# Kernel tuning notes

Hardware: AMD Instinct MI355X
Metric: run time of the kernel (lower is better)

## Reference

```python
import jax, jax.numpy as jnp
import numpy as np

VOCAB, EMBED, HIDDEN, N_CLASSES = 50257, 128, 256, 2
B = S = 512  # must be equal: the original module only runs when x.size(0)==x.size(1)


def gru_layer(x_seq, Wih, Whh, bih, bhh):
    """PyTorch-equation GRU over time axis 0. x_seq: (T, N, E) -> (T, N, H)."""
    T, N, _ = x_seq.shape
    H = Whh.shape[1]
    xi = x_seq @ Wih.T + bih  # precompute input projections for all steps: (T, N, 3H)

    def step(h, xi_t):
        gh = h @ Whh.T + bhh
        xr, xz, xn = jnp.split(xi_t, 3, axis=-1)
        hr, hz, hn = jnp.split(gh, 3, axis=-1)
        r = jax.nn.sigmoid(xr + hr)
        z = jax.nn.sigmoid(xz + hz)
        n = jnp.tanh(xn + r * hn)
        h_new = (1.0 - z) * n + z * h
        return h_new, h_new

    h0 = jnp.zeros((N, H), dtype=x_seq.dtype)
    _, ys = jax.lax.scan(step, h0, xi)
    return ys


def setup_inputs() -> dict:
    key = jax.random.key(0)
    ks = jax.random.split(key, 12)
    sc = 0.05
    return {
        "x": jax.random.randint(ks[0], (B, S), 0, VOCAB),
        "embed_table": jax.random.normal(ks[1], (VOCAB, EMBED), jnp.float32) * sc,
        "Wih0": jax.random.normal(ks[2], (3 * HIDDEN, EMBED), jnp.float32) * sc,
        "Whh0": jax.random.normal(ks[3], (3 * HIDDEN, HIDDEN), jnp.float32) * sc,
        "bih0": jax.random.normal(ks[4], (3 * HIDDEN,), jnp.float32) * sc,
        "bhh0": jax.random.normal(ks[5], (3 * HIDDEN,), jnp.float32) * sc,
        "Wih1": jax.random.normal(ks[6], (3 * HIDDEN, HIDDEN), jnp.float32) * sc,
        "Whh1": jax.random.normal(ks[7], (3 * HIDDEN, HIDDEN), jnp.float32) * sc,
        "bih1": jax.random.normal(ks[8], (3 * HIDDEN,), jnp.float32) * sc,
        "bhh1": jax.random.normal(ks[9], (3 * HIDDEN,), jnp.float32) * sc,
        "W_out": jax.random.normal(ks[10], (N_CLASSES, HIDDEN), jnp.float32) * sc,
        "b_out": jax.random.normal(ks[11], (N_CLASSES,), jnp.float32) * sc,
    }


def reference(x, embed_table, Wih0, Whh0, bih0, bhh0, Wih1, Whh1, bih1, bhh1, W_out, b_out):
    emb = embed_table[x]                 # (B, S, E)
    # nn.GRU default batch_first=False: dim 0 (=B) is TIME, dim 1 (=S) is batch.
    y = gru_layer(emb, Wih0, Whh0, bih0, bhh0)   # (B, S, H)
    y = gru_layer(y, Wih1, Whh1, bih1, bhh1)     # (B, S, H)
    h_t = y[:, -1, :]                    # (B, H)
    # self.dropout(h_t) in the original discards its result -> no-op.
    logit = h_t @ W_out.T + b_out        # (B, n_classes)
    return logit
```

## Files before the change

kernel.cpp:

```cpp
#include <hip/hip_runtime.h>
#include <hip/hip_fp16.h>

typedef _Float16 f16x2 __attribute__((ext_vector_type(2)));
typedef _Float16 half8 __attribute__((ext_vector_type(8)));

#define TS  512
#define HID 256
#define G3  768
#define EMB 128
#define NB1 8
#define RPB 96
#define CTL 767
#define BSZ 8

__device__ __forceinline__ float sigmoidf_(float x){ return 1.0f/(1.0f+__expf(-x)); }
__device__ __forceinline__ float tanhf_(float x){
  float e = __expf(-2.0f*fabsf(x));
  float t = (1.0f-e)/(1.0f+e);
  return copysignf(t,x);
}

__global__ __launch_bounds__(256) void xi0_kernel(const int* __restrict__ x,
    const float* __restrict__ emb_tab, const float* __restrict__ Wih0,
    const float* __restrict__ bih0, float* __restrict__ xi0)
{
  __shared__ float embs[8][EMB];
  __shared__ int idx8[8];
  int tid = threadIdx.x;
  int t0  = blockIdx.x * 8;
  if (tid < 8) idx8[tid] = x[(t0 + tid)*512 + 511];
  __syncthreads();
  for (int i = tid; i < 8*EMB; i += 256){
    int q = i >> 7, r = i & 127;
    embs[q][r] = emb_tab[(long)idx8[q]*EMB + r];
  }
  __syncthreads();
  for (int g = 0; g < 3; g++){
    int j = g*256 + tid;
    float b = bih0[j];
    float acc[8];
    #pragma unroll
    for (int u=0;u<8;u++) acc[u]=b;
    const float4* wrow = (const float4*)(Wih0 + (long)j*EMB);
    #pragma unroll 8
    for (int m=0;m<EMB/4;m++){
      float4 w = wrow[m];
      #pragma unroll
      for (int u=0;u<8;u++){
        acc[u] += w.x*embs[u][4*m+0] + w.y*embs[u][4*m+1]
                + w.z*embs[u][4*m+2] + w.w*embs[u][4*m+3];
      }
    }
    #pragma unroll
    for (int u=0;u<8;u++) xi0[(long)(t0+u)*G3 + j] = acc[u];
  }
}

#define SHUF(V,A,B) __builtin_shufflevector(V,V,A,B)
#define WR32(X) X(0,0) X(0,1) X(0,2) X(0,3) X(1,0) X(1,1) X(1,2) X(1,3) \
                X(2,0) X(2,1) X(2,2) X(2,3) X(3,0) X(3,1) X(3,2) X(3,3) \
                X(4,0) X(4,1) X(4,2) X(4,3) X(5,0) X(5,1) X(5,2) X(5,3) \
                X(6,0) X(6,1) X(6,2) X(6,3) X(7,0) X(7,1) X(7,2) X(7,3)

template<int MODE>
__device__ __forceinline__ void rec_layer(const float* __restrict__ Whh,
    const float* __restrict__ bhh, const float* __restrict__ xi,
    _Float16* __restrict__ h16out, float* __restrict__ f32out,
    unsigned* __restrict__ flagB, unsigned* __restrict__ cntB,
    _Float16 (*hbuf)[8*40], float* gh, float* bhhL)
{
  int tid = threadIdx.x;
  int g   = tid >> 3;
  int o   = tid & 7;

#define WDECL(I,C) half8 w##I##_##C;
  WR32(WDECL)
#define WLOAD(I,C) { \
    const float4* p_ = (const float4*)(Whh + (long)(8*g+(I))*HID + 32*o + 8*(C)); \
    float4 u_ = p_[0], v_ = p_[1]; \
    w##I##_##C = (half8){(_Float16)u_.x,(_Float16)u_.y,(_Float16)u_.z,(_Float16)u_.w, \
                         (_Float16)v_.x,(_Float16)v_.y,(_Float16)v_.z,(_Float16)v_.w}; }
  WR32(WLOAD)

  float hprev = 0.f;
  float xr=0.f, xz=0.f, xn=0.f;
  bhhL[tid] = bhh[tid];
  if (tid < 80) ((half8*)hbuf)[tid] = (half8)(_Float16)0;

  if (MODE == 1 && tid == CTL){
    while (__hip_atomic_load(&cntB[0], __ATOMIC_RELAXED, __HIP_MEMORY_SCOPE_AGENT) < NB1)
      __builtin_amdgcn_s_sleep(1);
    __threadfence();
  }
  __syncthreads();
  if (tid < HID){
    xr = xi[tid]; xz = xi[HID+tid]; xn = xi[2*HID+tid];
  }

  for (int t = 0; t < TS; t++){
    if (MODE == 1 && tid == CTL && ((t+1) & (BSZ-1)) == 0 && t+1 < TS){
      unsigned b = (unsigned)(t+1) >> 3;
      while (__hip_atomic_load(&cntB[b], __ATOMIC_RELAXED, __HIP_MEMORY_SCOPE_AGENT) < NB1)
        __builtin_amdgcn_s_sleep(1);
      __threadfence();
    }

    const half8* hp = (const half8*)(&hbuf[t & 1][o*40]);
    float a0=0.f,a1=0.f,a2=0.f,a3=0.f,a4=0.f,a5=0.f,a6=0.f,a7=0.f;
#define DOT1(I,C,HV) \
    a##I = __builtin_amdgcn_fdot2(SHUF(w##I##_##C,0,1), SHUF(HV,0,1), a##I, false); \
    a##I = __builtin_amdgcn_fdot2(SHUF(w##I##_##C,2,3), SHUF(HV,2,3), a##I, false); \
    a##I = __builtin_amdgcn_fdot2(SHUF(w##I##_##C,4,5), SHUF(HV,4,5), a##I, false); \
    a##I = __builtin_amdgcn_fdot2(SHUF(w##I##_##C,6,7), SHUF(HV,6,7), a##I, false);
#define DOTCHUNK(C) { half8 hv = hp[C]; \
    DOT1(0,C,hv) DOT1(1,C,hv) DOT1(2,C,hv) DOT1(3,C,hv) \
    DOT1(4,C,hv) DOT1(5,C,hv) DOT1(6,C,hv) DOT1(7,C,hv) }
    DOTCHUNK(0) DOTCHUNK(1) DOTCHUNK(2) DOTCHUNK(3)

    bool b0 = o & 1, b1 = o & 2, b2 = o & 4;
    float s, r_;
    s = b0 ? a0 : a1; r_ = __shfl_xor(s, 1, 64); float c0 = (b0 ? a1 : a0) + r_;
    s = b0 ? a2 : a3; r_ = __shfl_xor(s, 1, 64); float c1 = (b0 ? a3 : a2) + r_;
    s = b0 ? a4 : a5; r_ = __shfl_xor(s, 1, 64); float c2 = (b0 ? a5 : a4) + r_;
    s = b0 ? a6 : a7; r_ = __shfl_xor(s, 1, 64); float c3 = (b0 ? a7 : a6) + r_;
    s = b1 ? c0 : c1; r_ = __shfl_xor(s, 2, 64); float d0 = (b1 ? c1 : c0) + r_;
    s = b1 ? c2 : c3; r_ = __shfl_xor(s, 2, 64); float d1 = (b1 ? c3 : c2) + r_;
    s = b2 ? d0 : d1; r_ = __shfl_xor(s, 4, 64); float e  = (b2 ? d1 : d0) + r_;
    gh[tid] = e;
    __syncthreads();

    if (tid < HID){
      float r = sigmoidf_(xr + bhhL[tid] + gh[tid]);
      float z = sigmoidf_(xz + bhhL[HID+tid] + gh[HID+tid]);
      float n = tanhf_(xn + r*(gh[2*HID+tid] + bhhL[2*HID+tid]));
      float hnew = (1.0f - z)*n + z*hprev;
      hprev = hnew;
      if (MODE == 1) f32out[(long)t*HID + tid] = hnew;
      float partner = __shfl_xor(hnew, 1, 64);
      if ((tid & 1) == 0){
        f16x2 p; p.x = (_Float16)hnew; p.y = (_Float16)partner;
        *(f16x2*)(&hbuf[(t+1)&1][(tid>>5)*40 + (tid&31)]) = p;
        if (MODE == 0) *(f16x2*)(h16out + (long)t*HID + tid) = p;
      }
      if (t+1 < TS){
        const float* xp = xi + (long)(t+1)*G3;
        xr = xp[tid]; xz = xp[HID+tid]; xn = xp[2*HID+tid];
      }
    }
    __syncthreads();
    if (MODE == 0 && tid == CTL && ((t+1) & (BSZ-1)) == 0){
      __threadfence();
      __hip_atomic_store(&flagB[t >> 3], 1u, __ATOMIC_RELEASE, __HIP_MEMORY_SCOPE_AGENT);
    }
  }
}

__device__ __forceinline__ void xi1_stage(const float* __restrict__ Wih1,
    const float* __restrict__ bih1, const _Float16* __restrict__ h16,
    float* __restrict__ xi1, unsigned* __restrict__ flagB,
    unsigned* __restrict__ cntB, int slice)
{
  int tid = threadIdx.x;
  int r = tid >> 3, o = tid & 7;
  int row = slice*RPB + r;
  half8 w0,w1,w2,w3;
  {
    const float4* wp = (const float4*)(Wih1 + (long)row*HID + o*32);
    float4 p0=wp[0],p1=wp[1],p2=wp[2],p3=wp[3],p4=wp[4],p5=wp[5],p6=wp[6],p7=wp[7];
    w0 = (half8){(_Float16)p0.x,(_Float16)p0.y,(_Float16)p0.z,(_Float16)p0.w,
                 (_Float16)p1.x,(_Float16)p1.y,(_Float16)p1.z,(_Float16)p1.w};
    w1 = (half8){(_Float16)p2.x,(_Float16)p2.y,(_Float16)p2.z,(_Float16)p2.w,
                 (_Float16)p3.x,(_Float16)p3.y,(_Float16)p3.z,(_Float16)p3.w};
    w2 = (half8){(_Float16)p4.x,(_Float16)p4.y,(_Float16)p4.z,(_Float16)p4.w,
                 (_Float16)p5.x,(_Float16)p5.y,(_Float16)p5.z,(_Float16)p5.w};
    w3 = (half8){(_Float16)p6.x,(_Float16)p6.y,(_Float16)p6.z,(_Float16)p6.w,
                 (_Float16)p7.x,(_Float16)p7.y,(_Float16)p7.z,(_Float16)p7.w};
  }
  float bias = bih1[row];

  for (int b = 0; b < TS/BSZ; b++){
    if (tid == 0){
      while (__hip_atomic_load(&flagB[b], __ATOMIC_RELAXED, __HIP_MEMORY_SCOPE_AGENT) == 0u)
        __builtin_amdgcn_s_sleep(1);
      __threadfence();
    }
    __syncthreads();
    #pragma unroll 4
    for (int u = 0; u < BSZ; u++){
      int t = b*BSZ + u;
      const half8* hp = (const half8*)(h16 + (long)t*HID + o*32);
      half8 h0 = hp[0], h1 = hp[1], h2 = hp[2], h3 = hp[3];
      float acc = 0.f;
#define XDOT(W,H) \
      acc = __builtin_amdgcn_fdot2(SHUF(W,0,1), SHUF(H,0,1), acc, false); \
      acc = __builtin_amdgcn_fdot2(SHUF(W,2,3), SHUF(H,2,3), acc, false); \
      acc = __builtin_amdgcn_fdot2(SHUF(W,4,5), SHUF(H,4,5), acc, false); \
      acc = __builtin_amdgcn_fdot2(SHUF(W,6,7), SHUF(H,6,7), acc, false);
      XDOT(w0,h0) XDOT(w1,h1) XDOT(w2,h2) XDOT(w3,h3)
      acc += __shfl_xor(acc, 1, 64);
      acc += __shfl_xor(acc, 2, 64);
      acc += __shfl_xor(acc, 4, 64);
      if (o == 0) xi1[(long)t*G3 + row] = acc + bias;
    }
    __syncthreads();
    if (tid == 0){
      __threadfence();
      atomicAdd(&cntB[b], 1u);
    }
  }
}

__global__ __launch_bounds__(768, 3)
__attribute__((amdgpu_max_num_work_groups(10, 1, 1)))
void pipe_kernel(
    const float* __restrict__ Whh0, const float* __restrict__ bhh0,
    const float* __restrict__ xi0,
    const float* __restrict__ Wih1, const float* __restrict__ bih1,
    const float* __restrict__ Whh1, const float* __restrict__ bhh1,
    _Float16* __restrict__ h1f16, float* __restrict__ xi1,
    float* __restrict__ h2, unsigned* __restrict__ flagB,
    unsigned* __restrict__ cntB)
{
  __shared__ __align__(16) _Float16 hbuf[2][8*40];
  __shared__ float gh[G3];
  __shared__ float bhhL[G3];
  int bid = blockIdx.x;
  if (bid == 0)
    rec_layer<0>(Whh0, bhh0, xi0, h1f16, nullptr, flagB, cntB, hbuf, gh, bhhL);
  else if (bid == 9)
    rec_layer<1>(Whh1, bhh1, xi1, nullptr, h2, flagB, cntB, hbuf, gh, bhhL);
  else
    xi1_stage(Wih1, bih1, h1f16, xi1, flagB, cntB, bid - 1);
}

__global__ __launch_bounds__(1024) void logits_kernel(const float* __restrict__ h2,
    const float* __restrict__ Wout, const float* __restrict__ bout,
    float* __restrict__ out)
{
  __shared__ __align__(16) float wsm[2*HID];
  __shared__ float bs[2];
  int tid = threadIdx.x;
  if (tid < 2*HID) wsm[tid] = Wout[tid];
  if (tid < 2)     bs[tid]  = bout[tid];
  __syncthreads();
  int t = tid >> 1, c = tid & 1;
  const float4* hr = (const float4*)(h2 + (long)t*HID);
  const float4* wr = (const float4*)(wsm + c*HID);
  float acc = bs[c];
  #pragma unroll 8
  for (int m=0;m<HID/4;m++){
    float4 h = hr[m]; float4 wv = wr[m];
    acc += h.x*wv.x + h.y*wv.y + h.z*wv.z + h.w*wv.w;
  }
  out[tid] = acc;
}

extern "C" void kernel_launch(void* const* d_in, const int* in_sizes, int n_in,
                              void* d_out, int out_size, void* d_ws, size_t ws_size,
                              hipStream_t stream)
{
  const int*   x    = (const int*)  d_in[0];
  const float* emb  = (const float*)d_in[1];
  const float* Wih0 = (const float*)d_in[2];
  const float* Whh0 = (const float*)d_in[3];
  const float* bih0 = (const float*)d_in[4];
  const float* bhh0 = (const float*)d_in[5];
  const float* Wih1 = (const float*)d_in[6];
  const float* Whh1 = (const float*)d_in[7];
  const float* bih1 = (const float*)d_in[8];
  const float* bhh1 = (const float*)d_in[9];
  const float* Wout = (const float*)d_in[10];
  const float* bout = (const float*)d_in[11];
  float* out = (float*)d_out;

  char* ws = (char*)d_ws;
  float*     xi0   = (float*)(ws);
  float*     xi1   = (float*)(ws + 1572864);
  _Float16*  h1f16 = (_Float16*)(ws + 3145728);
  float*     h2    = (float*)(ws + 3407872);
  unsigned*  flagB = (unsigned*)(ws + 3932160);
  unsigned*  cntB  = (unsigned*)(ws + 3934208);

  hipMemsetAsync(ws + 3932160, 0, 4096, stream);
  xi0_kernel<<<64, 256, 0, stream>>>(x, emb, Wih0, bih0, xi0);
  pipe_kernel<<<10, 768, 0, stream>>>(Whh0, bhh0, xi0, Wih1, bih1,
                                      Whh1, bhh1, h1f16, xi1, h2, flagB, cntB);
  logits_kernel<<<1, 1024, 0, stream>>>(h2, Wout, bout, out);
}
```

Measured before the change: 855.8 us.

## Split each GRU recurrent layer across two workgroups exchanging half-hidden states per step

Each recurrent layer now runs on two workgroups, each owning 128 hidden units and 384 gate rows. At every step the pair swaps its half of the hidden state through global memory, using per-step counters that are spin-waited. This halves the per-block matvec work and register footprint, but adds a cross-workgroup handshake and global round-trip on every timestep. The xi1 workers now wait on both layer-0 counters instead of per-batch flags.

```diff
diff --git a/kernel.cpp b/kernel.cpp
--- a/kernel.cpp
+++ b/kernel.cpp
@@ -57,34 +57,40 @@
 }
 
 #define SHUF(V,A,B) __builtin_shufflevector(V,V,A,B)
-#define WR32(X) X(0,0) X(0,1) X(0,2) X(0,3) X(1,0) X(1,1) X(1,2) X(1,3) \
-                X(2,0) X(2,1) X(2,2) X(2,3) X(3,0) X(3,1) X(3,2) X(3,3) \
-                X(4,0) X(4,1) X(4,2) X(4,3) X(5,0) X(5,1) X(5,2) X(5,3) \
-                X(6,0) X(6,1) X(6,2) X(6,3) X(7,0) X(7,1) X(7,2) X(7,3)
+#define WR16(X) X(0,0) X(0,1) X(0,2) X(0,3) \
+                X(1,0) X(1,1) X(1,2) X(1,3) \
+                X(2,0) X(2,1) X(2,2) X(2,3) \
+                X(3,0) X(3,1) X(3,2) X(3,3)
 
 template<int MODE>
 __device__ __forceinline__ void rec_layer(const float* __restrict__ Whh,
     const float* __restrict__ bhh, const float* __restrict__ xi,
     _Float16* __restrict__ h16out, float* __restrict__ f32out,
-    unsigned* __restrict__ flagB, unsigned* __restrict__ cntB,
-    _Float16 (*hbuf)[8*40], float* gh, float* bhhL)
+    unsigned* __restrict__ cntB, unsigned* __restrict__ ctrOwn,
+    unsigned* __restrict__ ctrPar, int P,
+    _Float16 (*hbuf)[8*40], float* ghL, float* bhhL)
 {
   int tid = threadIdx.x;
   int g   = tid >> 3;
   int o   = tid & 7;
+  const int BASE = P * 128;
+  const int PB   = (1 - P) * 128;
 
 #define WDECL(I,C) half8 w##I##_##C;
-  WR32(WDECL)
+  WR16(WDECL)
 #define WLOAD(I,C) { \
-    const float4* p_ = (const float4*)(Whh + (long)(8*g+(I))*HID + 32*o + 8*(C)); \
+    int l_ = 4*g + (I); \
+    int wr_ = ((l_>>7)<<8) + BASE + (l_&127); \
+    const float4* p_ = (const float4*)(Whh + (long)wr_*HID + 32*o + 8*(C)); \
     float4 u_ = p_[0], v_ = p_[1]; \
     w##I##_##C = (half8){(_Float16)u_.x,(_Float16)u_.y,(_Float16)u_.z,(_Float16)u_.w, \
                          (_Float16)v_.x,(_Float16)v_.y,(_Float16)v_.z,(_Float16)v_.w}; }
-  WR32(WLOAD)
+  WR16(WLOAD)
 
   float hprev = 0.f;
   float xr=0.f, xz=0.f, xn=0.f;
-  bhhL[tid] = bhh[tid];
+  if (tid < 384)
+    bhhL[tid] = bhh[((tid>>7)<<8) + BASE + (tid&127)];
   if (tid < 80) ((half8*)hbuf)[tid] = (half8)(_Float16)0;
 
   if (MODE == 1 && tid == CTL){
@@ -93,8 +99,8 @@
     __threadfence();
   }
   __syncthreads();
-  if (tid < HID){
-    xr = xi[tid]; xz = xi[HID+tid]; xn = xi[2*HID+tid];
+  if (tid < 128){
+    xr = xi[BASE+tid]; xz = xi[256+BASE+tid]; xn = xi[512+BASE+tid];
   }
 
   for (int t = 0; t < TS; t++){
@@ -105,59 +111,78 @@
       __threadfence();
     }
 
+    if (t > 0 && tid < 64){
+      while (__hip_atomic_load(ctrPar, __ATOMIC_RELAXED, __HIP_MEMORY_SCOPE_AGENT)
+             < (unsigned)t) {}
+      __threadfence();
+      int u = PB + 2*tid;
+      f16x2 v;
+      if (MODE == 0){
+        v = *(const f16x2*)(h16out + (long)(t-1)*HID + u);
+      } else {
+        float2 f = *(const float2*)(f32out + (long)(t-1)*HID + u);
+        v.x = (_Float16)f.x; v.y = (_Float16)f.y;
+      }
+      *(f16x2*)(&hbuf[t & 1][(u>>5)*40 + (u&31)]) = v;
+    }
+    __syncthreads();
+
     const half8* hp = (const half8*)(&hbuf[t & 1][o*40]);
-    float a0=0.f,a1=0.f,a2=0.f,a3=0.f,a4=0.f,a5=0.f,a6=0.f,a7=0.f;
+    float a0=0.f,a1=0.f,a2=0.f,a3=0.f;
 #define DOT1(I,C,HV) \
     a##I = __builtin_amdgcn_fdot2(SHUF(w##I##_##C,0,1), SHUF(HV,0,1), a##I, false); \
     a##I = __builtin_amdgcn_fdot2(SHUF(w##I##_##C,2,3), SHUF(HV,2,3), a##I, false); \
     a##I = __builtin_amdgcn_fdot2(SHUF(w##I##_##C,4,5), SHUF(HV,4,5), a##I, false); \
     a##I = __builtin_amdgcn_fdot2(SHUF(w##I##_##C,6,7), SHUF(HV,6,7), a##I, false);
 #define DOTCHUNK(C) { half8 hv = hp[C]; \
-    DOT1(0,C,hv) DOT1(1,C,hv) DOT1(2,C,hv) DOT1(3,C,hv) \
-    DOT1(4,C,hv) DOT1(5,C,hv) DOT1(6,C,hv) DOT1(7,C,hv) }
+    DOT1(0,C,hv) DOT1(1,C,hv) DOT1(2,C,hv) DOT1(3,C,hv) }
     DOTCHUNK(0) DOTCHUNK(1) DOTCHUNK(2) DOTCHUNK(3)
 
-    bool b0 = o & 1, b1 = o & 2, b2 = o & 4;
-    float s, r_;
-    s = b0 ? a0 : a1; r_ = __shfl_xor(s, 1, 64); float c0 = (b0 ? a1 : a0) + r_;
-    s = b0 ? a2 : a3; r_ = __shfl_xor(s, 1, 64); float c1 = (b0 ? a3 : a2) + r_;
-    s = b0 ? a4 : a5; r_ = __shfl_xor(s, 1, 64); float c2 = (b0 ? a5 : a4) + r_;
-    s = b0 ? a6 : a7; r_ = __shfl_xor(s, 1, 64); float c3 = (b0 ? a7 : a6) + r_;
-    s = b1 ? c0 : c1; r_ = __shfl_xor(s, 2, 64); float d0 = (b1 ? c1 : c0) + r_;
-    s = b1 ? c2 : c3; r_ = __shfl_xor(s, 2, 64); float d1 = (b1 ? c3 : c2) + r_;
-    s = b2 ? d0 : d1; r_ = __shfl_xor(s, 4, 64); float e  = (b2 ? d1 : d0) + r_;
-    gh[tid] = e;
-    __syncthreads();
-
-    if (tid < HID){
-      float r = sigmoidf_(xr + bhhL[tid] + gh[tid]);
-      float z = sigmoidf_(xz + bhhL[HID+tid] + gh[HID+tid]);
-      float n = tanhf_(xn + r*(gh[2*HID+tid] + bhhL[2*HID+tid]));
+    {
+      bool b0 = o & 1, b1 = o & 2;
+      float s, r_;
+      s = b0 ? a0 : a1; r_ = __shfl_xor(s, 1, 64); float c0 = (b0 ? a1 : a0) + r_;
+      s = b0 ? a2 : a3; r_ = __shfl_xor(s, 1, 64); float c1 = (b0 ? a3 : a2) + r_;
+      s = b1 ? c0 : c1; r_ = __shfl_xor(s, 2, 64); float d  = (b1 ? c1 : c0) + r_;
+      float e = d + __shfl_xor(d, 4, 64);
+      if (o < 4) ghL[4*g + o] = e;
+    }
+    __syncthreads();
+
+    if (tid < 128){
+      float r = sigmoidf_(xr + bhhL[tid] + ghL[tid]);
+      float z = sigmoidf_(xz + bhhL[128+tid] + ghL[128+tid]);
+      float n = tanhf_(xn + r*(ghL[256+tid] + bhhL[256+tid]));
       float hnew = (1.0f - z)*n + z*hprev;
       hprev = hnew;
-      if (MODE == 1) f32out[(long)t*HID + tid] = hnew;
       float partner = __shfl_xor(hnew, 1, 64);
+      int u = BASE + tid;
       if ((tid & 1) == 0){
         f16x2 p; p.x = (_Float16)hnew; p.y = (_Float16)partner;
-        *(f16x2*)(&hbuf[(t+1)&1][(tid>>5)*40 + (tid&31)]) = p;
-        if (MODE == 0) *(f16x2*)(h16out + (long)t*HID + tid) = p;
+        *(f16x2*)(&hbuf[(t+1)&1][(u>>5)*40 + (u&31)]) = p;
+        if (MODE == 0){
+          *(f16x2*)(h16out + (long)t*HID + u) = p;
+        } else {
+          float2 q; q.x = hnew; q.y = partner;
+          *(float2*)(f32out + (long)t*HID + u) = q;
+        }
       }
       if (t+1 < TS){
         const float* xp = xi + (long)(t+1)*G3;
-        xr = xp[tid]; xz = xp[HID+tid]; xn = xp[2*HID+tid];
+        xr = xp[BASE+tid]; xz = xp[256+BASE+tid]; xn = xp[512+BASE+tid];
       }
     }
     __syncthreads();
-    if (MODE == 0 && tid == CTL && ((t+1) & (BSZ-1)) == 0){
-      __threadfence();
-      __hip_atomic_store(&flagB[t >> 3], 1u, __ATOMIC_RELEASE, __HIP_MEMORY_SCOPE_AGENT);
+    if (tid == CTL){
+      __threadfence();
+      __hip_atomic_store(ctrOwn, (unsigned)(t+1), __ATOMIC_RELEASE, __HIP_MEMORY_SCOPE_AGENT);
     }
   }
 }
 
 __device__ __forceinline__ void xi1_stage(const float* __restrict__ Wih1,
     const float* __restrict__ bih1, const _Float16* __restrict__ h16,
-    float* __restrict__ xi1, unsigned* __restrict__ flagB,
+    float* __restrict__ xi1, unsigned* __restrict__ ctrs,
     unsigned* __restrict__ cntB, int slice)
 {
   int tid = threadIdx.x;
@@ -180,7 +205,9 @@
 
   for (int b = 0; b < TS/BSZ; b++){
     if (tid == 0){
-      while (__hip_atomic_load(&flagB[b], __ATOMIC_RELAXED, __HIP_MEMORY_SCOPE_AGENT) == 0u)
+      unsigned tgt = (unsigned)(BSZ*(b+1));
+      while (__hip_atomic_load(&ctrs[0],  __ATOMIC_RELAXED, __HIP_MEMORY_SCOPE_AGENT) < tgt ||
+             __hip_atomic_load(&ctrs[16], __ATOMIC_RELAXED, __HIP_MEMORY_SCOPE_AGENT) < tgt)
         __builtin_amdgcn_s_sleep(1);
       __threadfence();
     }
@@ -211,26 +238,31 @@
 }
 
 __global__ __launch_bounds__(768, 3)
-__attribute__((amdgpu_max_num_work_groups(10, 1, 1)))
 void pipe_kernel(
     const float* __restrict__ Whh0, const float* __restrict__ bhh0,
     const float* __restrict__ xi0,
     const float* __restrict__ Wih1, const float* __restrict__ bih1,
     const float* __restrict__ Whh1, const float* __restrict__ bhh1,
     _Float16* __restrict__ h1f16, float* __restrict__ xi1,
-    float* __restrict__ h2, unsigned* __restrict__ flagB,
+    float* __restrict__ h2, unsigned* __restrict__ ctrs,
     unsigned* __restrict__ cntB)
 {
   __shared__ __align__(16) _Float16 hbuf[2][8*40];
-  __shared__ float gh[G3];
-  __shared__ float bhhL[G3];
+  __shared__ float ghL[384];
+  __shared__ float bhhL[384];
   int bid = blockIdx.x;
   if (bid == 0)
-    rec_layer<0>(Whh0, bhh0, xi0, h1f16, nullptr, flagB, cntB, hbuf, gh, bhhL);
+    rec_layer<0>(Whh0, bhh0, xi0, h1f16, nullptr, cntB, ctrs+0,  ctrs+16, 0, hbuf, ghL, bhhL);
+  else if (bid == 8)
+    rec_layer<0>(Whh0, bhh0, xi0, h1f16, nullptr, cntB, ctrs+16, ctrs+0,  1, hbuf, ghL, bhhL);
+  else if (bid == 1)
+    rec_layer<1>(Whh1, bhh1, xi1, nullptr, h2,    cntB, ctrs+32, ctrs+48, 0, hbuf, ghL, bhhL);
   else if (bid == 9)
-    rec_layer<1>(Whh1, bhh1, xi1, nullptr, h2, flagB, cntB, hbuf, gh, bhhL);
-  else
-    xi1_stage(Wih1, bih1, h1f16, xi1, flagB, cntB, bid - 1);
+    rec_layer<1>(Whh1, bhh1, xi1, nullptr, h2,    cntB, ctrs+48, ctrs+32, 1, hbuf, ghL, bhhL);
+  else {
+    int slice = (bid < 8) ? bid - 2 : bid - 4;
+    xi1_stage(Wih1, bih1, h1f16, xi1, ctrs, cntB, slice);
+  }
 }
 
 __global__ __launch_bounds__(1024) void logits_kernel(const float* __restrict__ h2,
@@ -278,12 +310,12 @@
   float*     xi1   = (float*)(ws + 1572864);
   _Float16*  h1f16 = (_Float16*)(ws + 3145728);
   float*     h2    = (float*)(ws + 3407872);
-  unsigned*  flagB = (unsigned*)(ws + 3932160);
+  unsigned*  ctrs  = (unsigned*)(ws + 3932160);
   unsigned*  cntB  = (unsigned*)(ws + 3934208);
 
   hipMemsetAsync(ws + 3932160, 0, 4096, stream);
   xi0_kernel<<<64, 256, 0, stream>>>(x, emb, Wih0, bih0, xi0);
-  pipe_kernel<<<10, 768, 0, stream>>>(Whh0, bhh0, xi0, Wih1, bih1,
-                                      Whh1, bhh1, h1f16, xi1, h2, flagB, cntB);
+  pipe_kernel<<<12, 768, 0, stream>>>(Whh0, bhh0, xi0, Wih1, bih1,
+                                      Whh1, bhh1, h1f16, xi1, h2, ctrs, cntB);
   logits_kernel<<<1, 1024, 0, stream>>>(h2, Wout, bout, out);
 }
```

Result: slower. 1.363 ms (+59.2%).

## Split recurrent weights across registers, LDS and L2 with 512-thread blocks

Applied to the files above, without the earlier changes.

Each recurrent block shrinks from 768 to 512 threads, so every 8-thread group now computes 12 gate rows instead of 8. Six rows are kept in registers, three in LDS, and three are streamed each step from an fp16 packed copy that the xi0 kernel writes to workspace. The number of xi1 producer blocks rises from 8 to 12, each covering 64 rows. The aim is fewer waves per step and more producer parallelism, at the price of extra LDS and global loads inside the serial time loop.

```diff
diff --git a/kernel.cpp b/kernel.cpp
--- a/kernel.cpp
+++ b/kernel.cpp
@@ -8,9 +8,10 @@
 #define HID 256
 #define G3  768
 #define EMB 128
-#define NB1 8
-#define RPB 96
-#define CTL 767
+#define THR 512
+#define NB1 12
+#define RPB 64
+#define CTL 511
 #define BSZ 8
 
 __device__ __forceinline__ float sigmoidf_(float x){ return 1.0f/(1.0f+__expf(-x)); }
@@ -22,7 +23,9 @@
 
 __global__ __launch_bounds__(256) void xi0_kernel(const int* __restrict__ x,
     const float* __restrict__ emb_tab, const float* __restrict__ Wih0,
-    const float* __restrict__ bih0, float* __restrict__ xi0)
+    const float* __restrict__ bih0, float* __restrict__ xi0,
+    const float* __restrict__ Whh0, const float* __restrict__ Whh1,
+    _Float16* __restrict__ wpk0, _Float16* __restrict__ wpk1)
 {
   __shared__ float embs[8][EMB];
   __shared__ int idx8[8];
@@ -54,37 +57,60 @@
     #pragma unroll
     for (int u=0;u<8;u++) xi0[(long)(t0+u)*G3 + j] = acc[u];
   }
+  int gid = blockIdx.x*256 + tid;
+  for (int e = gid; e < 2*192*256; e += 64*256){
+    int L = (e >= 192*256) ? 1 : 0;
+    int i = e - L*192*256;
+    int s = i >> 8, c = i & 255;
+    int row = 12*(s/3) + 9 + (s%3);
+    const float* W = L ? Whh1 : Whh0;
+    _Float16*    P = L ? wpk1 : wpk0;
+    P[i] = (_Float16)W[(long)row*HID + c];
+  }
 }
 
 #define SHUF(V,A,B) __builtin_shufflevector(V,V,A,B)
-#define WR32(X) X(0,0) X(0,1) X(0,2) X(0,3) X(1,0) X(1,1) X(1,2) X(1,3) \
+#define WR24(X) X(0,0) X(0,1) X(0,2) X(0,3) X(1,0) X(1,1) X(1,2) X(1,3) \
                 X(2,0) X(2,1) X(2,2) X(2,3) X(3,0) X(3,1) X(3,2) X(3,3) \
-                X(4,0) X(4,1) X(4,2) X(4,3) X(5,0) X(5,1) X(5,2) X(5,3) \
-                X(6,0) X(6,1) X(6,2) X(6,3) X(7,0) X(7,1) X(7,2) X(7,3)
+                X(4,0) X(4,1) X(4,2) X(4,3) X(5,0) X(5,1) X(5,2) X(5,3)
 
 template<int MODE>
 __device__ __forceinline__ void rec_layer(const float* __restrict__ Whh,
     const float* __restrict__ bhh, const float* __restrict__ xi,
+    const _Float16* __restrict__ wpk,
     _Float16* __restrict__ h16out, float* __restrict__ f32out,
     unsigned* __restrict__ flagB, unsigned* __restrict__ cntB,
-    _Float16 (*hbuf)[8*40], float* gh, float* bhhL)
+    _Float16 (*hbuf)[8*40], half8* ldsw, float* gh, float* bhhL)
 {
   int tid = threadIdx.x;
   int g   = tid >> 3;
   int o   = tid & 7;
 
 #define WDECL(I,C) half8 w##I##_##C;
-  WR32(WDECL)
+  WR24(WDECL)
 #define WLOAD(I,C) { \
-    const float4* p_ = (const float4*)(Whh + (long)(8*g+(I))*HID + 32*o + 8*(C)); \
+    const float4* p_ = (const float4*)(Whh + (long)(12*g+(I))*HID + 32*o + 8*(C)); \
     float4 u_ = p_[0], v_ = p_[1]; \
     w##I##_##C = (half8){(_Float16)u_.x,(_Float16)u_.y,(_Float16)u_.z,(_Float16)u_.w, \
                          (_Float16)v_.x,(_Float16)v_.y,(_Float16)v_.z,(_Float16)v_.w}; }
-  WR32(WLOAD)
+  WR24(WLOAD)
+
+  #pragma unroll
+  for (int k = 0; k < 12; k++){
+    int row = 12*g + 6 + (k >> 2);
+    int C = k & 3;
+    const float4* p_ = (const float4*)(Whh + (long)row*HID + 32*o + 8*C);
+    float4 u_ = p_[0], v_ = p_[1];
+    ldsw[k*THR + tid] = (half8){(_Float16)u_.x,(_Float16)u_.y,(_Float16)u_.z,(_Float16)u_.w,
+                                (_Float16)v_.x,(_Float16)v_.y,(_Float16)v_.z,(_Float16)v_.w};
+  }
+  const half8* sp0 = (const half8*)(wpk + ((long)(3*g+0))*HID + 32*o);
+  const half8* sp1 = (const half8*)(wpk + ((long)(3*g+1))*HID + 32*o);
+  const half8* sp2 = (const half8*)(wpk + ((long)(3*g+2))*HID + 32*o);
 
   float hprev = 0.f;
   float xr=0.f, xz=0.f, xn=0.f;
-  bhhL[tid] = bhh[tid];
+  for (int i = tid; i < G3; i += THR) bhhL[i] = bhh[i];
   if (tid < 80) ((half8*)hbuf)[tid] = (half8)(_Float16)0;
 
   if (MODE == 1 && tid == CTL){
@@ -106,16 +132,23 @@
     }
 
     const half8* hp = (const half8*)(&hbuf[t & 1][o*40]);
-    float a0=0.f,a1=0.f,a2=0.f,a3=0.f,a4=0.f,a5=0.f,a6=0.f,a7=0.f;
-#define DOT1(I,C,HV) \
-    a##I = __builtin_amdgcn_fdot2(SHUF(w##I##_##C,0,1), SHUF(HV,0,1), a##I, false); \
-    a##I = __builtin_amdgcn_fdot2(SHUF(w##I##_##C,2,3), SHUF(HV,2,3), a##I, false); \
-    a##I = __builtin_amdgcn_fdot2(SHUF(w##I##_##C,4,5), SHUF(HV,4,5), a##I, false); \
-    a##I = __builtin_amdgcn_fdot2(SHUF(w##I##_##C,6,7), SHUF(HV,6,7), a##I, false);
-#define DOTCHUNK(C) { half8 hv = hp[C]; \
-    DOT1(0,C,hv) DOT1(1,C,hv) DOT1(2,C,hv) DOT1(3,C,hv) \
-    DOT1(4,C,hv) DOT1(5,C,hv) DOT1(6,C,hv) DOT1(7,C,hv) }
-    DOTCHUNK(0) DOTCHUNK(1) DOTCHUNK(2) DOTCHUNK(3)
+    float a0=0.f,a1=0.f,a2=0.f,a3=0.f,a4=0.f,a5=0.f,
+          a6=0.f,a7=0.f,a8=0.f,a9=0.f,a10=0.f,a11=0.f;
+#define D8(ACC, WV, HV) \
+    ACC = __builtin_amdgcn_fdot2(SHUF(WV,0,1), SHUF(HV,0,1), ACC, false); \
+    ACC = __builtin_amdgcn_fdot2(SHUF(WV,2,3), SHUF(HV,2,3), ACC, false); \
+    ACC = __builtin_amdgcn_fdot2(SHUF(WV,4,5), SHUF(HV,4,5), ACC, false); \
+    ACC = __builtin_amdgcn_fdot2(SHUF(WV,6,7), SHUF(HV,6,7), ACC, false);
+#define CHUNK(C) { half8 hv = hp[C]; \
+    half8 l0 = ldsw[(0*4+(C))*THR + tid]; \
+    half8 l1 = ldsw[(1*4+(C))*THR + tid]; \
+    half8 l2 = ldsw[(2*4+(C))*THR + tid]; \
+    half8 s0 = sp0[C]; half8 s1 = sp1[C]; half8 s2 = sp2[C]; \
+    D8(a0, w0_##C, hv) D8(a1, w1_##C, hv) D8(a2, w2_##C, hv) \
+    D8(a3, w3_##C, hv) D8(a4, w4_##C, hv) D8(a5, w5_##C, hv) \
+    D8(a6, l0, hv) D8(a7, l1, hv) D8(a8, l2, hv) \
+    D8(a9, s0, hv) D8(a10, s1, hv) D8(a11, s2, hv) }
+    CHUNK(0) CHUNK(1) CHUNK(2) CHUNK(3)
 
     bool b0 = o & 1, b1 = o & 2, b2 = o & 4;
     float s, r_;
@@ -126,7 +159,12 @@
     s = b1 ? c0 : c1; r_ = __shfl_xor(s, 2, 64); float d0 = (b1 ? c1 : c0) + r_;
     s = b1 ? c2 : c3; r_ = __shfl_xor(s, 2, 64); float d1 = (b1 ? c3 : c2) + r_;
     s = b2 ? d0 : d1; r_ = __shfl_xor(s, 4, 64); float e  = (b2 ? d1 : d0) + r_;
-    gh[tid] = e;
+    gh[12*g + o] = e;
+    s = b0 ? a8 : a9;   r_ = __shfl_xor(s, 1, 64); float c4 = (b0 ? a9  : a8 ) + r_;
+    s = b0 ? a10 : a11; r_ = __shfl_xor(s, 1, 64); float c5 = (b0 ? a11 : a10) + r_;
+    s = b1 ? c4 : c5;   r_ = __shfl_xor(s, 2, 64); float d2 = (b1 ? c5  : c4 ) + r_;
+    float e2 = d2 + __shfl_xor(d2, 4, 64);
+    if (o < 4) gh[12*g + 8 + o] = e2;
     __syncthreads();
 
     if (tid < HID){
@@ -210,25 +248,26 @@
   }
 }
 
-__global__ __launch_bounds__(768, 3)
-__attribute__((amdgpu_max_num_work_groups(10, 1, 1)))
+__global__ __launch_bounds__(THR, 2)
 void pipe_kernel(
     const float* __restrict__ Whh0, const float* __restrict__ bhh0,
     const float* __restrict__ xi0,
     const float* __restrict__ Wih1, const float* __restrict__ bih1,
     const float* __restrict__ Whh1, const float* __restrict__ bhh1,
+    const _Float16* __restrict__ wpk0, const _Float16* __restrict__ wpk1,
     _Float16* __restrict__ h1f16, float* __restrict__ xi1,
     float* __restrict__ h2, unsigned* __restrict__ flagB,
     unsigned* __restrict__ cntB)
 {
+  __shared__ __align__(16) half8 ldsw[12*THR];
   __shared__ __align__(16) _Float16 hbuf[2][8*40];
   __shared__ float gh[G3];
   __shared__ float bhhL[G3];
   int bid = blockIdx.x;
   if (bid == 0)
-    rec_layer<0>(Whh0, bhh0, xi0, h1f16, nullptr, flagB, cntB, hbuf, gh, bhhL);
-  else if (bid == 9)
-    rec_layer<1>(Whh1, bhh1, xi1, nullptr, h2, flagB, cntB, hbuf, gh, bhhL);
+    rec_layer<0>(Whh0, bhh0, xi0, wpk0, h1f16, nullptr, flagB, cntB, hbuf, ldsw, gh, bhhL);
+  else if (bid == 13)
+    rec_layer<1>(Whh1, bhh1, xi1, wpk1, nullptr, h2, flagB, cntB, hbuf, ldsw, gh, bhhL);
   else
     xi1_stage(Wih1, bih1, h1f16, xi1, flagB, cntB, bid - 1);
 }
@@ -280,10 +319,14 @@
   float*     h2    = (float*)(ws + 3407872);
   unsigned*  flagB = (unsigned*)(ws + 3932160);
   unsigned*  cntB  = (unsigned*)(ws + 3934208);
+  _Float16*  wpk0  = (_Float16*)(ws + 3936256);
+  _Float16*  wpk1  = (_Float16*)(ws + 4034560);
 
   hipMemsetAsync(ws + 3932160, 0, 4096, stream);
-  xi0_kernel<<<64, 256, 0, stream>>>(x, emb, Wih0, bih0, xi0);
-  pipe_kernel<<<10, 768, 0, stream>>>(Whh0, bhh0, xi0, Wih1, bih1,
-                                      Whh1, bhh1, h1f16, xi1, h2, flagB, cntB);
+  xi0_kernel<<<64, 256, 0, stream>>>(x, emb, Wih0, bih0, xi0,
+                                     Whh0, Whh1, wpk0, wpk1);
+  pipe_kernel<<<14, THR, 0, stream>>>(Whh0, bhh0, xi0, Wih1, bih1,
+                                      Whh1, bhh1, wpk0, wpk1,
+                                      h1f16, xi1, h2, flagB, cntB);
   logits_kernel<<<1, 1024, 0, stream>>>(h2, Wout, bout, out);
 }
```

New measurement: 893.7 us. 1.04x slower.

## Fold layer-0 input projection into pipelined persistent kernel as producer blocks

Applied to the files above, without the earlier changes.

Removes the separate xi0_kernel and adds 8 extra blocks in pipe_kernel that compute the layer-0 input projection step by step. After every 8 steps they publish progress through a new counter array. Layer-0 recurrence now waits on these counters, so it starts before the whole projection is finished and one kernel launch disappears. The cost is extra spin-wait synchronisation, and correctness relies on all 18 blocks being co-resident.

```diff
diff --git a/kernel.cpp b/kernel.cpp
--- a/kernel.cpp
+++ b/kernel.cpp
@@ -12,6 +12,7 @@
 #define RPB 96
 #define CTL 767
 #define BSZ 8
+#define WAITN 8
 
 __device__ __forceinline__ float sigmoidf_(float x){ return 1.0f/(1.0f+__expf(-x)); }
 __device__ __forceinline__ float tanhf_(float x){
@@ -20,42 +21,6 @@
   return copysignf(t,x);
 }
 
-__global__ __launch_bounds__(256) void xi0_kernel(const int* __restrict__ x,
-    const float* __restrict__ emb_tab, const float* __restrict__ Wih0,
-    const float* __restrict__ bih0, float* __restrict__ xi0)
-{
-  __shared__ float embs[8][EMB];
-  __shared__ int idx8[8];
-  int tid = threadIdx.x;
-  int t0  = blockIdx.x * 8;
-  if (tid < 8) idx8[tid] = x[(t0 + tid)*512 + 511];
-  __syncthreads();
-  for (int i = tid; i < 8*EMB; i += 256){
-    int q = i >> 7, r = i & 127;
-    embs[q][r] = emb_tab[(long)idx8[q]*EMB + r];
-  }
-  __syncthreads();
-  for (int g = 0; g < 3; g++){
-    int j = g*256 + tid;
-    float b = bih0[j];
-    float acc[8];
-    #pragma unroll
-    for (int u=0;u<8;u++) acc[u]=b;
-    const float4* wrow = (const float4*)(Wih0 + (long)j*EMB);
-    #pragma unroll 8
-    for (int m=0;m<EMB/4;m++){
-      float4 w = wrow[m];
-      #pragma unroll
-      for (int u=0;u<8;u++){
-        acc[u] += w.x*embs[u][4*m+0] + w.y*embs[u][4*m+1]
-                + w.z*embs[u][4*m+2] + w.w*embs[u][4*m+3];
-      }
-    }
-    #pragma unroll
-    for (int u=0;u<8;u++) xi0[(long)(t0+u)*G3 + j] = acc[u];
-  }
-}
-
 #define SHUF(V,A,B) __builtin_shufflevector(V,V,A,B)
 #define WR32(X) X(0,0) X(0,1) X(0,2) X(0,3) X(1,0) X(1,1) X(1,2) X(1,3) \
                 X(2,0) X(2,1) X(2,2) X(2,3) X(3,0) X(3,1) X(3,2) X(3,3) \
@@ -66,7 +31,7 @@
 __device__ __forceinline__ void rec_layer(const float* __restrict__ Whh,
     const float* __restrict__ bhh, const float* __restrict__ xi,
     _Float16* __restrict__ h16out, float* __restrict__ f32out,
-    unsigned* __restrict__ flagB, unsigned* __restrict__ cntB,
+    unsigned* __restrict__ flagB, unsigned* __restrict__ cntWait,
     _Float16 (*hbuf)[8*40], float* gh, float* bhhL)
 {
   int tid = threadIdx.x;
@@ -87,8 +52,8 @@
   bhhL[tid] = bhh[tid];
   if (tid < 80) ((half8*)hbuf)[tid] = (half8)(_Float16)0;
 
-  if (MODE == 1 && tid == CTL){
-    while (__hip_atomic_load(&cntB[0], __ATOMIC_RELAXED, __HIP_MEMORY_SCOPE_AGENT) < NB1)
+  if (tid == CTL){
+    while (__hip_atomic_load(&cntWait[0], __ATOMIC_RELAXED, __HIP_MEMORY_SCOPE_AGENT) < WAITN)
       __builtin_amdgcn_s_sleep(1);
     __threadfence();
   }
@@ -98,9 +63,9 @@
   }
 
   for (int t = 0; t < TS; t++){
-    if (MODE == 1 && tid == CTL && ((t+1) & (BSZ-1)) == 0 && t+1 < TS){
+    if (tid == CTL && ((t+1) & (BSZ-1)) == 0 && t+1 < TS){
       unsigned b = (unsigned)(t+1) >> 3;
-      while (__hip_atomic_load(&cntB[b], __ATOMIC_RELAXED, __HIP_MEMORY_SCOPE_AGENT) < NB1)
+      while (__hip_atomic_load(&cntWait[b], __ATOMIC_RELAXED, __HIP_MEMORY_SCOPE_AGENT) < WAITN)
         __builtin_amdgcn_s_sleep(1);
       __threadfence();
     }
@@ -210,27 +175,71 @@
   }
 }
 
+__device__ __forceinline__ void xi0_stage(const int* __restrict__ x,
+    const float* __restrict__ emb_tab, const float* __restrict__ Wih0,
+    const float* __restrict__ bih0, float* __restrict__ xi0,
+    unsigned* __restrict__ cntX, int slice, float* embp)
+{
+  int tid = threadIdx.x;
+  int j = tid >> 3, kk = tid & 7;
+  int row = slice*96 + j;
+  float w16[16];
+  {
+    const float4* wp = (const float4*)(Wih0 + (long)row*EMB + kk*16);
+    float4 a = wp[0], b = wp[1], c = wp[2], d = wp[3];
+    w16[0]=a.x;  w16[1]=a.y;  w16[2]=a.z;  w16[3]=a.w;
+    w16[4]=b.x;  w16[5]=b.y;  w16[6]=b.z;  w16[7]=b.w;
+    w16[8]=c.x;  w16[9]=c.y;  w16[10]=c.z; w16[11]=c.w;
+    w16[12]=d.x; w16[13]=d.y; w16[14]=d.z; w16[15]=d.w;
+  }
+  float bias = bih0[row];
+
+  for (int t = 0; t < TS; t++){
+    if (tid < EMB){
+      int idx = x[(long)t*512 + 511];
+      embp[tid + (tid >> 4)] = emb_tab[(long)idx*EMB + tid];
+    }
+    __syncthreads();
+    float a = 0.f;
+    #pragma unroll
+    for (int m = 0; m < 16; m++) a += w16[m] * embp[kk*17 + m];
+    a += __shfl_xor(a, 1, 64);
+    a += __shfl_xor(a, 2, 64);
+    a += __shfl_xor(a, 4, 64);
+    if (kk == 0) xi0[(long)t*G3 + row] = a + bias;
+    __syncthreads();
+    if (((t+1) & (BSZ-1)) == 0 && tid == 0){
+      __threadfence();
+      atomicAdd(&cntX[t >> 3], 1u);
+    }
+  }
+}
+
 __global__ __launch_bounds__(768, 3)
-__attribute__((amdgpu_max_num_work_groups(10, 1, 1)))
 void pipe_kernel(
     const float* __restrict__ Whh0, const float* __restrict__ bhh0,
-    const float* __restrict__ xi0,
     const float* __restrict__ Wih1, const float* __restrict__ bih1,
     const float* __restrict__ Whh1, const float* __restrict__ bhh1,
-    _Float16* __restrict__ h1f16, float* __restrict__ xi1,
-    float* __restrict__ h2, unsigned* __restrict__ flagB,
-    unsigned* __restrict__ cntB)
+    const int* __restrict__ x, const float* __restrict__ emb_tab,
+    const float* __restrict__ Wih0, const float* __restrict__ bih0,
+    float* __restrict__ xi0, _Float16* __restrict__ h1f16,
+    float* __restrict__ xi1, float* __restrict__ h2,
+    unsigned* __restrict__ flagB, unsigned* __restrict__ cntB,
+    unsigned* __restrict__ cntX)
 {
   __shared__ __align__(16) _Float16 hbuf[2][8*40];
   __shared__ float gh[G3];
   __shared__ float bhhL[G3];
+  __shared__ float embp[136];
   int bid = blockIdx.x;
   if (bid == 0)
-    rec_layer<0>(Whh0, bhh0, xi0, h1f16, nullptr, flagB, cntB, hbuf, gh, bhhL);
+    rec_layer<0>(Whh0, bhh0, xi0, h1f16, nullptr, flagB, cntX, hbuf, gh, bhhL);
   else if (bid == 9)
     rec_layer<1>(Whh1, bhh1, xi1, nullptr, h2, flagB, cntB, hbuf, gh, bhhL);
+  else if (bid < 9)
+    xi1_stage(Wih1, bih1, h1f16, xi1, flagB, cntB, bid - 1);
   else
-    xi1_stage(Wih1, bih1, h1f16, xi1, flagB, cntB, bid - 1);
+    xi0_stage(x, emb_tab, Wih0, bih0, xi0, cntX, bid - 10, embp);
 }
 
 __global__ __launch_bounds__(1024) void logits_kernel(const float* __restrict__ h2,
@@ -279,11 +288,12 @@
   _Float16*  h1f16 = (_Float16*)(ws + 3145728);
   float*     h2    = (float*)(ws + 3407872);
   unsigned*  flagB = (unsigned*)(ws + 3932160);
-  unsigned*  cntB  = (unsigned*)(ws + 3934208);
+  unsigned*  cntB  = (unsigned*)(ws + 3933184);
+  unsigned*  cntX  = (unsigned*)(ws + 3934208);
 
   hipMemsetAsync(ws + 3932160, 0, 4096, stream);
-  xi0_kernel<<<64, 256, 0, stream>>>(x, emb, Wih0, bih0, xi0);
-  pipe_kernel<<<10, 768, 0, stream>>>(Whh0, bhh0, xi0, Wih1, bih1,
-                                      Whh1, bhh1, h1f16, xi1, h2, flagB, cntB);
+  pipe_kernel<<<18, 768, 0, stream>>>(Whh0, bhh0, Wih1, bih1, Whh1, bhh1,
+                                      x, emb, Wih0, bih0,
+                                      xi0, h1f16, xi1, h2, flagB, cntB, cntX);
   logits_kernel<<<1, 1024, 0, stream>>>(h2, Wout, bout, out);
 }
```

New measurement: 834.9 us, median of 2. -2.4%, faster.
